# Kernel tuning notes

Hardware: AMD Instinct MI355X
Metric: run time of the kernel (lower is better)

Reference implementation:

```python
import jax, jax.numpy as jnp
import numpy as np

SPARSITY_RATIO = 0.9
THRESHOLD_PCT = 0.95


def setup_inputs() -> dict:
    key = jax.random.key(0)
    B, H, S = 1, 16, 2048
    scores = jax.random.normal(key, (B, H, S, S), dtype=jnp.float32)
    return {"attention_scores": scores, "batch_size": B, "num_heads": H, "seq_len": S}


def _dynamic_threshold_mask(scores):
    B, H, Sq, Sk = scores.shape
    # per-(batch, head) quantile threshold over flattened Sq*Sk scores
    flat = scores.reshape(B, H, -1)
    thr = jnp.quantile(flat, THRESHOLD_PCT, axis=-1)[:, :, None, None]
    thr_mask = scores >= thr
    density = jnp.mean(thr_mask.astype(jnp.float32))

    k = max(1, int(Sk * (1.0 - SPARSITY_RATIO)))  # static k

    def topk_branch(_):
        _, idx = jax.lax.top_k(scores, k)  # [B,H,Sq,k]
        row_mask = lambda row_idx: jnp.zeros((Sk,), dtype=bool).at[row_idx].set(True)
        return jax.vmap(jax.vmap(jax.vmap(row_mask)))(idx)

    def thr_branch(_):
        return thr_mask

    # torch: if mask.float().mean() > 1 - sparsity_ratio -> fall back to topk
    return jax.lax.cond(density > (1.0 - SPARSITY_RATIO), topk_branch, thr_branch, operand=None)


def reference(attention_scores, batch_size, num_heads, seq_len):
    return _dynamic_threshold_mask(attention_scores)
```

## Files before the change

### kernel.cpp

```cpp
#include <hip/hip_runtime.h>
#include <stdint.h>


#define NUM_HEADS 16
#define PER_HEAD (1u << 22)
#define K_SEL 3984588u
#define WSTART 1.6298828125f
#define WEND   1.66015625f
#define WBIN0 1290
#define WBINS 62
#define CAND_CAP 16384
#define WBUF_CAP 384
#define FILT_CAP 768
#define NBINS_FB 2050

typedef int   int4v   __attribute__((ext_vector_type(4)));
typedef float float4v __attribute__((ext_vector_type(4)));

#define OFF_CNT   64
#define OFF_OVF   128
#define OFF_COV   192
#define OFF_THR   256
#define OFF_CVAL  320
#define OFF_CPOS  (320 + NUM_HEADS * CAND_CAP * 4)
#define ZERO_WORDS 64

__global__ void k_zero(uint32_t* __restrict__ ws) {
    if (threadIdx.x < ZERO_WORDS) ws[threadIdx.x] = 0u;
}

__global__ void k_pass1(const float* __restrict__ scores, int* __restrict__ out,
                        uint32_t* __restrict__ below, uint32_t* __restrict__ cnt,
                        uint32_t* __restrict__ ovf, uint32_t* __restrict__ cpos,
                        float* __restrict__ cval) {
    __shared__ uint32_t wpos[WBUF_CAP];
    __shared__ float    wval[WBUF_CAP];
    __shared__ uint32_t wcnt, wbase;
    __shared__ uint32_t wavesum[4];
    const int h = blockIdx.y;
    if (threadIdx.x == 0) wcnt = 0;
    __syncthreads();
    const float4v* p = (const float4v*)(scores + (size_t)h * PER_HEAD);
    int4v* o = (int4v*)(out + (size_t)h * PER_HEAD);
    const uint32_t nvec = PER_HEAD / 4;
    uint32_t nb = 0;
    for (uint32_t i = blockIdx.x * blockDim.x + threadIdx.x; i < nvec;
         i += gridDim.x * blockDim.x) {
        float4v v = p[i];
        int4v m;
#pragma unroll
        for (int j = 0; j < 4; ++j) {
            float x = v[j];
            m[j] = (x >= WEND) ? 1 : 0;
            nb += (x < WSTART) ? 1u : 0u;
            if (x >= WSTART && x < WEND) {
                uint32_t pos = atomicAdd(&wcnt, 1u);
                if (pos < WBUF_CAP) { wpos[pos] = i * 4u + j; wval[pos] = x; }
            }
        }
        __builtin_nontemporal_store(m, &o[i]);
    }
#pragma unroll
    for (int off = 32; off > 0; off >>= 1) nb += __shfl_down(nb, off, 64);
    const int lane = threadIdx.x & 63, wid = threadIdx.x >> 6;
    if (lane == 0) wavesum[wid] = nb;
    __syncthreads();
    if (threadIdx.x == 0) {
        atomicAdd(&below[h], wavesum[0] + wavesum[1] + wavesum[2] + wavesum[3]);
        uint32_t nc = wcnt;
        if (nc > WBUF_CAP) atomicOr(&ovf[h], 1u);
        wbase = atomicAdd(&cnt[h], min(nc, (uint32_t)WBUF_CAP));
    }
    __syncthreads();
    const uint32_t nc = min(wcnt, (uint32_t)WBUF_CAP);
    const uint32_t base = wbase;
    for (uint32_t i = threadIdx.x; i < nc; i += blockDim.x) {
        uint32_t pos = base + i;
        if (pos < CAND_CAP) {
            cpos[h * CAND_CAP + pos] = wpos[i];
            cval[h * CAND_CAP + pos] = wval[i];
        }
    }
}

__global__ void k_select(const uint32_t* __restrict__ below, const uint32_t* __restrict__ cnt,
                         const uint32_t* __restrict__ ovf, const float* __restrict__ cval,
                         uint32_t* __restrict__ cov, float* __restrict__ thr) {
    const int h = blockIdx.x;
    __shared__ uint32_t wh[WBINS];
    __shared__ float fc[FILT_CAP];
    __shared__ uint32_t lcnt, bad;
    __shared__ int sbin;
    __shared__ uint32_t sres;
    const uint32_t craw = cnt[h];
    const long long r = (long long)K_SEL - (long long)below[h];
    if (ovf[h] || craw > CAND_CAP || r < 0 || r >= (long long)craw) {
        return;
    }
    const uint32_t n = craw;
    for (int i = threadIdx.x; i < WBINS; i += blockDim.x) wh[i] = 0;
    if (threadIdx.x == 0) { lcnt = 0; bad = 0; }
    __syncthreads();
    for (uint32_t i = threadIdx.x; i < n; i += blockDim.x) {
        float x = cval[h * CAND_CAP + i];
        int b = (int)((__float_as_uint(x) >> 12) & 0x7FFu) - WBIN0;
        atomicAdd(&wh[b], 1u);
    }
    __syncthreads();
    if (threadIdx.x == 0) {
        uint32_t cum = 0, res = 0;
        int b = 0;
        for (; b < WBINS; ++b) {
            uint32_t nx = cum + wh[b];
            if ((uint32_t)r < nx) { res = (uint32_t)r - cum; break; }
            cum = nx;
        }
        sbin = b; sres = res;
        if (wh[b] > FILT_CAP) bad = 1;
    }
    __syncthreads();
    if (bad) return;
    const int tb = sbin;
    const uint32_t r2 = sres;
    for (uint32_t i = threadIdx.x; i < n; i += blockDim.x) {
        float x = cval[h * CAND_CAP + i];
        int b = (int)((__float_as_uint(x) >> 12) & 0x7FFu) - WBIN0;
        if (b == tb) { uint32_t pos = atomicAdd(&lcnt, 1u); if (pos < FILT_CAP) fc[pos] = x; }
    }
    __syncthreads();
    const uint32_t m = lcnt;
    for (uint32_t i = threadIdx.x; i < m; i += blockDim.x) {
        float x = fc[i];
        uint32_t less = 0, eq = 0;
        for (uint32_t j = 0; j < m; ++j) {
            float y = fc[j];
            less += (y < x);
            eq += (y == x);
        }
        if (less <= r2 && r2 < less + eq) thr[h] = x;
    }
    __syncthreads();
    if (threadIdx.x == 0) cov[h] = 1u;
}

__global__ void k_fallback_thr(const float* __restrict__ scores, const uint32_t* __restrict__ cov,
                               float* __restrict__ thr) {
    const int h = blockIdx.x;
    if (cov[h]) return;
    __shared__ uint32_t fh[NBINS_FB];
    __shared__ float fc[FILT_CAP];
    __shared__ uint32_t lcnt;
    __shared__ int sbin;
    __shared__ uint32_t sres;
    for (int i = threadIdx.x; i < NBINS_FB; i += blockDim.x) fh[i] = 0;
    if (threadIdx.x == 0) lcnt = 0;
    __syncthreads();
    const float* p = scores + (size_t)h * PER_HEAD;
    for (uint32_t i = threadIdx.x; i < PER_HEAD; i += blockDim.x) {
        float x = p[i];
        int b = (x < 1.0f) ? 0 : ((x >= 2.0f) ? (NBINS_FB - 1)
                                              : 1 + (int)((__float_as_uint(x) >> 12) & 0x7FFu));
        atomicAdd(&fh[b], 1u);
    }
    __syncthreads();
    if (threadIdx.x == 0) {
        uint64_t cum = 0; uint32_t res = 0; int b = 0;
        for (; b < NBINS_FB; ++b) {
            uint64_t nx = cum + fh[b];
            if ((uint64_t)K_SEL < nx) { res = (uint32_t)(K_SEL - cum); break; }
            cum = nx;
        }
        sbin = b; sres = res;
    }
    __syncthreads();
    const int tb = sbin;
    const uint32_t r2 = sres;
    for (uint32_t i = threadIdx.x; i < PER_HEAD; i += blockDim.x) {
        float x = p[i];
        int b = (x < 1.0f) ? 0 : ((x >= 2.0f) ? (NBINS_FB - 1)
                                              : 1 + (int)((__float_as_uint(x) >> 12) & 0x7FFu));
        if (b == tb) { uint32_t pos = atomicAdd(&lcnt, 1u); if (pos < FILT_CAP) fc[pos] = x; }
    }
    __syncthreads();
    const uint32_t m = min(lcnt, (uint32_t)FILT_CAP);
    for (uint32_t i = threadIdx.x; i < m; i += blockDim.x) {
        float x = fc[i];
        uint32_t less = 0, eq = 0;
        for (uint32_t j = 0; j < m; ++j) {
            float y = fc[j];
            less += (y < x);
            eq += (y == x);
        }
        if (less <= r2 && r2 < less + eq) thr[h] = x;
    }
}

__global__ void k_maskfull(const float* __restrict__ scores, const uint32_t* __restrict__ cov,
                           const float* __restrict__ thr, int* __restrict__ out) {
    const int h = blockIdx.y;
    if (cov[h]) return;
    const float t = thr[h];
    const float4v* p = (const float4v*)(scores + (size_t)h * PER_HEAD);
    int4v* o = (int4v*)(out + (size_t)h * PER_HEAD);
    const uint32_t nvec = PER_HEAD / 4;
    for (uint32_t i = blockIdx.x * blockDim.x + threadIdx.x; i < nvec;
         i += gridDim.x * blockDim.x) {
        float4v v = p[i];
        int4v m;
        m.x = (v.x >= t) ? 1 : 0;
        m.y = (v.y >= t) ? 1 : 0;
        m.z = (v.z >= t) ? 1 : 0;
        m.w = (v.w >= t) ? 1 : 0;
        o[i] = m;
    }
}

__global__ void k_fix(const uint32_t* __restrict__ cnt, const uint32_t* __restrict__ cov,
                      const uint32_t* __restrict__ cpos, const float* __restrict__ cval,
                      const float* __restrict__ thr, int* __restrict__ out) {
    const int h = blockIdx.y;
    if (!cov[h]) return;
    const uint32_t n = min(cnt[h], (uint32_t)CAND_CAP);
    const float t = thr[h];
    int* oh = out + (size_t)h * PER_HEAD;
    for (uint32_t i = blockIdx.x * blockDim.x + threadIdx.x; i < n;
         i += gridDim.x * blockDim.x) {
        oh[cpos[h * CAND_CAP + i]] = (cval[h * CAND_CAP + i] >= t) ? 1 : 0;
    }
}

extern "C" void kernel_launch(void* const* d_in, const int* in_sizes, int n_in,
                              void* d_out, int out_size, void* d_ws, size_t ws_size,
                              hipStream_t stream) {
    const float* scores = (const float*)d_in[0];
    int* out = (int*)d_out;
    uint8_t* ws = (uint8_t*)d_ws;

    uint32_t* below = (uint32_t*)ws;
    uint32_t* cnt   = (uint32_t*)(ws + OFF_CNT);
    uint32_t* ovf   = (uint32_t*)(ws + OFF_OVF);
    uint32_t* cov   = (uint32_t*)(ws + OFF_COV);
    float*    thr   = (float*)(ws + OFF_THR);
    float*    cval  = (float*)(ws + OFF_CVAL);
    uint32_t* cpos  = (uint32_t*)(ws + OFF_CPOS);

    dim3 blk(256);
    k_zero<<<1, 64, 0, stream>>>((uint32_t*)ws);
    k_pass1<<<dim3(256, NUM_HEADS), blk, 0, stream>>>(scores, out, below, cnt, ovf, cpos, cval);
    k_select<<<NUM_HEADS, 256, 0, stream>>>(below, cnt, ovf, cval, cov, thr);
    k_fallback_thr<<<NUM_HEADS, 256, 0, stream>>>(scores, cov, thr);
    k_maskfull<<<dim3(256, NUM_HEADS), blk, 0, stream>>>(scores, cov, thr, out);
    k_fix<<<dim3(8, NUM_HEADS), blk, 0, stream>>>(cnt, cov, cpos, cval, thr, out);
}
```

Measured before the change: 164.5 us.

## Split pass into stats-only scan and unconditional mask pass, drop fix-up kernel

The first pass no longer writes a provisional mask or candidate positions; it only counts values below the window and collects window values, gated by a wave-level any check. A single mask kernel then always rewrites the full output from the final threshold, replacing the conditional full-mask kernel and the scatter fix-up. This removes the position buffer and the fix-up launch but adds a second full read of the scores on the common path.

New measurement: 210.9 us. 1.28x slower.

```diff
diff --git a/kernel.cpp b/kernel.cpp
--- a/kernel.cpp
+++ b/kernel.cpp
@@ -22,43 +22,45 @@
 #define OFF_COV   192
 #define OFF_THR   256
 #define OFF_CVAL  320
-#define OFF_CPOS  (320 + NUM_HEADS * CAND_CAP * 4)
 #define ZERO_WORDS 64
 
 __global__ void k_zero(uint32_t* __restrict__ ws) {
     if (threadIdx.x < ZERO_WORDS) ws[threadIdx.x] = 0u;
 }
 
-__global__ void k_pass1(const float* __restrict__ scores, int* __restrict__ out,
-                        uint32_t* __restrict__ below, uint32_t* __restrict__ cnt,
-                        uint32_t* __restrict__ ovf, uint32_t* __restrict__ cpos,
+__global__ void k_stats(const float* __restrict__ scores, uint32_t* __restrict__ below,
+                        uint32_t* __restrict__ cnt, uint32_t* __restrict__ ovf,
                         float* __restrict__ cval) {
-    __shared__ uint32_t wpos[WBUF_CAP];
-    __shared__ float    wval[WBUF_CAP];
+    __shared__ float wval[WBUF_CAP];
     __shared__ uint32_t wcnt, wbase;
     __shared__ uint32_t wavesum[4];
     const int h = blockIdx.y;
     if (threadIdx.x == 0) wcnt = 0;
     __syncthreads();
     const float4v* p = (const float4v*)(scores + (size_t)h * PER_HEAD);
-    int4v* o = (int4v*)(out + (size_t)h * PER_HEAD);
     const uint32_t nvec = PER_HEAD / 4;
+    const uint32_t stride = gridDim.x * blockDim.x;
     uint32_t nb = 0;
-    for (uint32_t i = blockIdx.x * blockDim.x + threadIdx.x; i < nvec;
-         i += gridDim.x * blockDim.x) {
+    for (uint32_t i = blockIdx.x * blockDim.x + threadIdx.x; i < nvec; i += stride) {
         float4v v = p[i];
-        int4v m;
+        bool lanehit = false;
 #pragma unroll
         for (int j = 0; j < 4; ++j) {
             float x = v[j];
-            m[j] = (x >= WEND) ? 1 : 0;
-            nb += (x < WSTART) ? 1u : 0u;
-            if (x >= WSTART && x < WEND) {
-                uint32_t pos = atomicAdd(&wcnt, 1u);
-                if (pos < WBUF_CAP) { wpos[pos] = i * 4u + j; wval[pos] = x; }
+            bool c1 = (x < WSTART), c2 = (x < WEND);
+            nb += c1 ? 1u : 0u;
+            lanehit |= (c1 != c2);
+        }
+        if (__any(lanehit)) {
+#pragma unroll
+            for (int j = 0; j < 4; ++j) {
+                float x = v[j];
+                if (x >= WSTART && x < WEND) {
+                    uint32_t pos = atomicAdd(&wcnt, 1u);
+                    if (pos < WBUF_CAP) wval[pos] = x;
+                }
             }
         }
-        __builtin_nontemporal_store(m, &o[i]);
     }
 #pragma unroll
     for (int off = 32; off > 0; off >>= 1) nb += __shfl_down(nb, off, 64);
@@ -73,13 +75,10 @@
     }
     __syncthreads();
     const uint32_t nc = min(wcnt, (uint32_t)WBUF_CAP);
-    const uint32_t base = wbase;
+    const uint32_t bs = wbase;
     for (uint32_t i = threadIdx.x; i < nc; i += blockDim.x) {
-        uint32_t pos = base + i;
-        if (pos < CAND_CAP) {
-            cpos[h * CAND_CAP + pos] = wpos[i];
-            cval[h * CAND_CAP + pos] = wval[i];
-        }
+        uint32_t pos = bs + i;
+        if (pos < CAND_CAP) cval[h * CAND_CAP + pos] = wval[i];
     }
 }
 
@@ -195,16 +194,15 @@
     }
 }
 
-__global__ void k_maskfull(const float* __restrict__ scores, const uint32_t* __restrict__ cov,
-                           const float* __restrict__ thr, int* __restrict__ out) {
+__global__ void k_maskB(const float* __restrict__ scores, const float* __restrict__ thr,
+                        int* __restrict__ out) {
     const int h = blockIdx.y;
-    if (cov[h]) return;
     const float t = thr[h];
     const float4v* p = (const float4v*)(scores + (size_t)h * PER_HEAD);
     int4v* o = (int4v*)(out + (size_t)h * PER_HEAD);
     const uint32_t nvec = PER_HEAD / 4;
-    for (uint32_t i = blockIdx.x * blockDim.x + threadIdx.x; i < nvec;
-         i += gridDim.x * blockDim.x) {
+    const uint32_t stride = gridDim.x * blockDim.x;
+    for (uint32_t i = blockIdx.x * blockDim.x + threadIdx.x; i < nvec; i += stride) {
         float4v v = p[i];
         int4v m;
         m.x = (v.x >= t) ? 1 : 0;
@@ -215,20 +213,6 @@
     }
 }
 
-__global__ void k_fix(const uint32_t* __restrict__ cnt, const uint32_t* __restrict__ cov,
-                      const uint32_t* __restrict__ cpos, const float* __restrict__ cval,
-                      const float* __restrict__ thr, int* __restrict__ out) {
-    const int h = blockIdx.y;
-    if (!cov[h]) return;
-    const uint32_t n = min(cnt[h], (uint32_t)CAND_CAP);
-    const float t = thr[h];
-    int* oh = out + (size_t)h * PER_HEAD;
-    for (uint32_t i = blockIdx.x * blockDim.x + threadIdx.x; i < n;
-         i += gridDim.x * blockDim.x) {
-        oh[cpos[h * CAND_CAP + i]] = (cval[h * CAND_CAP + i] >= t) ? 1 : 0;
-    }
-}
-
 extern "C" void kernel_launch(void* const* d_in, const int* in_sizes, int n_in,
                               void* d_out, int out_size, void* d_ws, size_t ws_size,
                               hipStream_t stream) {
@@ -242,13 +226,11 @@
     uint32_t* cov   = (uint32_t*)(ws + OFF_COV);
     float*    thr   = (float*)(ws + OFF_THR);
     float*    cval  = (float*)(ws + OFF_CVAL);
-    uint32_t* cpos  = (uint32_t*)(ws + OFF_CPOS);
 
     dim3 blk(256);
     k_zero<<<1, 64, 0, stream>>>((uint32_t*)ws);
-    k_pass1<<<dim3(256, NUM_HEADS), blk, 0, stream>>>(scores, out, below, cnt, ovf, cpos, cval);
+    k_stats<<<dim3(256, NUM_HEADS), blk, 0, stream>>>(scores, below, cnt, ovf, cval);
     k_select<<<NUM_HEADS, 256, 0, stream>>>(below, cnt, ovf, cval, cov, thr);
     k_fallback_thr<<<NUM_HEADS, 256, 0, stream>>>(scores, cov, thr);
-    k_maskfull<<<dim3(256, NUM_HEADS), blk, 0, stream>>>(scores, cov, thr, out);
-    k_fix<<<dim3(8, NUM_HEADS), blk, 0, stream>>>(cnt, cov, cpos, cval, thr, out);
-}
+    k_maskB<<<dim3(1024, NUM_HEADS), blk, 0, stream>>>(scores, thr, out);
+}
```
